# Optimization experiments

Hardware: AMD Instinct MI355X
Metric: run time of the kernel (lower is better)

## Reference

```python
import jax, jax.numpy as jnp
import numpy as np

N = 8192
IN_F = 512
NFEAT = 512
OUT_F = 512


def setup_inputs() -> dict:
    key = jax.random.key(0)
    k1, k2, k3, k4, k5 = jax.random.split(key, 5)
    stdv = 1.0 / np.sqrt(OUT_F)
    return {
        "input": jax.random.normal(k1, (N, IN_F), dtype=jnp.float32),
        "adj": jax.random.uniform(k2, (N, N), dtype=jnp.float32),
        "x": jax.random.normal(k3, (N, NFEAT), dtype=jnp.float32),
        "weight": jax.random.uniform(k4, (IN_F + N + NFEAT, OUT_F), minval=-stdv, maxval=stdv, dtype=jnp.float32),
        "bias": jax.random.uniform(k5, (OUT_F,), minval=-stdv, maxval=stdv, dtype=jnp.float32),
    }


def reference(input, adj, x, weight, bias):
    # support = [adj @ input | adj | x]  -> [n, in_features + n + nfeat]
    support = jnp.concatenate((adj @ input, adj, x), axis=1)
    return support @ weight + bias
```

## Files before the change

kernel.cpp:

```cpp
#include <hip/hip_runtime.h>
#include <hip/hip_bf16.h>

typedef __attribute__((ext_vector_type(4))) float f32x4;
typedef __attribute__((ext_vector_type(8))) short bf16x8;
typedef __attribute__((ext_vector_type(4))) unsigned short u16x4;
typedef __attribute__((ext_vector_type(8))) unsigned short u16x8;

__device__ __forceinline__ unsigned short f2bf(float f) {
    unsigned int u = __builtin_bit_cast(unsigned int, f);
    u += 0x7fffu + ((u >> 16) & 1u);
    return (unsigned short)(u >> 16);
}

#define SWZ(i) ((i) ^ ((((i) >> 6) & 7) << 3))

__global__ void transpose_cvt(const float* __restrict__ src,
                              unsigned short* __restrict__ dst,
                              int rows, int cols) {
    int idx = blockIdx.x * 256 + threadIdx.x;
    int n = idx / rows;
    int k = idx - n * rows;
    unsigned short v = f2bf(src[(size_t)k * cols + n]);
    int tile = (n >> 7) * (rows >> 6) + (k >> 6);
    dst[(size_t)tile * 8192 + SWZ((n & 127) * 64 + (k & 63))] = v;
}

template<int EPI>
__global__ __launch_bounds__(512, 4)
void gemm_small(const float* __restrict__ A, long lda,
                const unsigned short* __restrict__ Bt,
                int K,
                const float* __restrict__ epi, long lde,
                const float* __restrict__ bias,
                void* __restrict__ Dptr, long ldd) {
    __shared__ unsigned short sA[2][64 * 64];
    __shared__ unsigned short sB[2][128 * 64];

    const int t = threadIdx.x;
    const int l = t & 63;
    const int w = t >> 6;
    const int wm = w >> 2;
    const int wn = w & 3;

    int mt, nt;
    {
        int lin = blockIdx.y * gridDim.x + blockIdx.x;
        int xcd = lin & 7;
        int slot = lin >> 3;
        int ppx = gridDim.y >> 3;
        mt = xcd * ppx + slot / gridDim.x;
        nt = slot % gridDim.x;
    }
    const long m0 = (long)mt * 64;
    const long n0 = (long)nt * 128;
    const int KT = K >> 6;
    const unsigned short* Bblk = Bt + (size_t)nt * KT * 8192;

    f32x4 acc[2][2];
    #pragma unroll
    for (int m = 0; m < 2; ++m)
        #pragma unroll
        for (int n = 0; n < 2; ++n)
            acc[m][n] = {0.f, 0.f, 0.f, 0.f};

    f32x4 aX0, aX1, aY0, aY1;

    auto gll_B = [&](int kt, int buf) {
        const unsigned short* src = Bblk + (size_t)kt * 8192 + t * 8;
        #pragma unroll
        for (int r = 0; r < 2; ++r)
            __builtin_amdgcn_global_load_lds(
                (const __attribute__((address_space(1))) void*)(src + r * 4096),
                (__attribute__((address_space(3))) void*)&sB[buf][r * 4096 + w * 512],
                16, 0, 0);
    };

    auto load_A = [&](int kt, f32x4& a0, f32x4& a1) {
        const float* p0 = &A[(m0 + (t >> 4)) * lda + (long)kt * 64 + ((t & 15) << 2)];
        const float* p1 = p0 + 32 * lda;
        asm volatile("global_load_dwordx4 %0, %2, off\n\t"
                     "global_load_dwordx4 %1, %3, off"
                     : "=&v"(a0), "=&v"(a1)
                     : "v"(p0), "v"(p1)
                     : "memory");
    };

    auto write_A = [&](int buf, const f32x4& a0, const f32x4& a1) {
        int e0 = t * 4;
        u16x4 w0 = {f2bf(a0[0]), f2bf(a0[1]), f2bf(a0[2]), f2bf(a0[3])};
        *reinterpret_cast<u16x4*>(&sA[buf][SWZ(e0)]) = w0;
        int e1 = 2048 + t * 4;
        u16x4 w1 = {f2bf(a1[0]), f2bf(a1[1]), f2bf(a1[2]), f2bf(a1[3])};
        *reinterpret_cast<u16x4*>(&sA[buf][SWZ(e1)]) = w1;
    };

    auto compute = [&](int buf) {
        #pragma unroll
        for (int kk = 0; kk < 2; ++kk) {
            bf16x8 af[2], bfr[2];
            const int kb = kk * 32 + ((l >> 4) << 3);
            #pragma unroll
            for (int m = 0; m < 2; ++m) {
                int row = wm * 32 + m * 16 + (l & 15);
                af[m] = *reinterpret_cast<const bf16x8*>(&sA[buf][SWZ(row * 64 + kb)]);
            }
            #pragma unroll
            for (int n = 0; n < 2; ++n) {
                int col = wn * 32 + n * 16 + (l & 15);
                bfr[n] = *reinterpret_cast<const bf16x8*>(&sB[buf][SWZ(col * 64 + kb)]);
            }
            __builtin_amdgcn_s_setprio(1);
            #pragma unroll
            for (int m = 0; m < 2; ++m)
                #pragma unroll
                for (int n = 0; n < 2; ++n)
                    acc[m][n] = __builtin_amdgcn_mfma_f32_16x16x32_bf16(
                        af[m], bfr[n], acc[m][n], 0, 0, 0);
            __builtin_amdgcn_s_setprio(0);
        }
    };

    gll_B(0, 0);
    load_A(0, aX0, aX1);
    load_A(1, aY0, aY1);
    asm volatile("s_waitcnt vmcnt(2)" ::: "memory");
    __builtin_amdgcn_sched_barrier(0);
    write_A(0, aX0, aX1);
    asm volatile("s_waitcnt lgkmcnt(0)" ::: "memory");
    __builtin_amdgcn_s_barrier();
    __builtin_amdgcn_sched_barrier(0);

    const int nk = K >> 6;
    for (int p = 0; p + 2 < nk; p += 2) {
        gll_B(p + 1, 1);
        load_A(p + 2, aX0, aX1);
        compute(0);
        asm volatile("s_waitcnt vmcnt(4)" ::: "memory");
        __builtin_amdgcn_sched_barrier(0);
        write_A(1, aY0, aY1);
        asm volatile("s_waitcnt vmcnt(2) lgkmcnt(0)" ::: "memory");
        __builtin_amdgcn_s_barrier();
        __builtin_amdgcn_sched_barrier(0);

        gll_B(p + 2, 0);
        load_A(p + 3, aY0, aY1);
        compute(1);
        asm volatile("s_waitcnt vmcnt(4)" ::: "memory");
        __builtin_amdgcn_sched_barrier(0);
        write_A(0, aX0, aX1);
        asm volatile("s_waitcnt vmcnt(2) lgkmcnt(0)" ::: "memory");
        __builtin_amdgcn_s_barrier();
        __builtin_amdgcn_sched_barrier(0);
    }

    gll_B(nk - 1, 1);
    compute(0);
    asm volatile("s_waitcnt vmcnt(2)" ::: "memory");
    __builtin_amdgcn_sched_barrier(0);
    write_A(1, aY0, aY1);
    asm volatile("s_waitcnt vmcnt(0) lgkmcnt(0)" ::: "memory");
    __builtin_amdgcn_s_barrier();
    __builtin_amdgcn_sched_barrier(0);
    compute(1);

    const int jrow = (l >> 4) * 4;
    #pragma unroll
    for (int m = 0; m < 2; ++m) {
        const long row = m0 + wm * 32 + m * 16 + jrow;
        #pragma unroll
        for (int n = 0; n < 2; ++n) {
            const long col = n0 + wn * 32 + n * 16 + (l & 15);
            f32x4 v = acc[m][n];
            if constexpr (EPI == 0) {
                u16x4 o;
                #pragma unroll
                for (int j = 0; j < 4; ++j)
                    o[j] = f2bf(v[j] + epi[(row + j) * lde + col]);
                int tile = ((int)col >> 8) * 256 + ((int)row >> 5);
                int e = ((int)col & 255) * 32 + ((int)row & 31);
                *reinterpret_cast<u16x4*>(
                    &((unsigned short*)Dptr)[(size_t)tile * 8192 + SWZ(e)]) = o;
            } else {
                float b = bias[col];
                #pragma unroll
                for (int j = 0; j < 4; ++j)
                    ((float*)Dptr)[(row + j) * ldd + col] = v[j] + b;
            }
        }
    }
}

__global__ __launch_bounds__(512, 4)
void gemm_big(const float* __restrict__ A,
              const unsigned short* __restrict__ Bt,
              float* __restrict__ Out) {
    __shared__ unsigned short sA[2][128 * 32];
    __shared__ unsigned short sB[2][256 * 32];

    const int t = threadIdx.x;
    const int l = t & 63;
    const int w = t >> 6;
    const int wm = w & 1;
    const int wn = w >> 1;

    const int lin = blockIdx.x;
    const int xcd = lin & 7;
    const int idx = lin >> 3;
    const int mt = xcd * 8 + (idx & 7);
    const int rest = idx >> 3;
    const int nt = rest & 1;
    const int kq = rest >> 1;

    const long m0 = (long)mt * 128;
    const long k0 = (long)kq * 2048;
    const int ktb = nt * 256 + kq * 64;
    constexpr int P = 64;

    f32x4 acc[4][4];
    #pragma unroll
    for (int mi = 0; mi < 4; ++mi)
        #pragma unroll
        for (int ni = 0; ni < 4; ++ni)
            acc[mi][ni] = {0.f, 0.f, 0.f, 0.f};

    f32x4 aX0, aX1, aY0, aY1;

    auto gll_B = [&](int p, int buf) {
        const unsigned short* src = Bt + (size_t)(ktb + p) * 8192 + t * 8;
        #pragma unroll
        for (int r = 0; r < 2; ++r)
            __builtin_amdgcn_global_load_lds(
                (const __attribute__((address_space(1))) void*)(src + r * 4096),
                (__attribute__((address_space(3))) void*)&sB[buf][r * 4096 + w * 512],
                16, 0, 0);
    };

    auto load_A = [&](int p, f32x4& a0, f32x4& a1) {
        const float* base = A + m0 * 8192 + k0 + (long)p * 32;
        const float* p0 = base + (long)(t >> 3) * 8192 + ((t & 7) << 2);
        const float* p1 = base + (long)(64 + (t >> 3)) * 8192 + ((t & 7) << 2);
        asm volatile("global_load_dwordx4 %0, %2, off\n\t"
                     "global_load_dwordx4 %1, %3, off"
                     : "=&v"(a0), "=&v"(a1)
                     : "v"(p0), "v"(p1)
                     : "memory");
    };

    auto write_A = [&](int buf, const f32x4& a0, const f32x4& a1) {
        int e0 = (t >> 3) * 32 + ((t & 7) << 2);
        int e1 = (64 + (t >> 3)) * 32 + ((t & 7) << 2);
        u16x4 w0 = {f2bf(a0[0]), f2bf(a0[1]), f2bf(a0[2]), f2bf(a0[3])};
        *reinterpret_cast<u16x4*>(&sA[buf][SWZ(e0)]) = w0;
        u16x4 w1 = {f2bf(a1[0]), f2bf(a1[1]), f2bf(a1[2]), f2bf(a1[3])};
        *reinterpret_cast<u16x4*>(&sA[buf][SWZ(e1)]) = w1;
    };

    auto compute = [&](int buf) {
        const int kb = (l >> 4) << 3;
        bf16x8 af[4], bfr[4];
        #pragma unroll
        for (int mi = 0; mi < 4; ++mi) {
            int row = wm * 64 + mi * 16 + (l & 15);
            af[mi] = *reinterpret_cast<const bf16x8*>(&sA[buf][SWZ(row * 32 + kb)]);
        }
        #pragma unroll
        for (int ni = 0; ni < 4; ++ni) {
            int col = wn * 64 + ni * 16 + (l & 15);
            bfr[ni] = *reinterpret_cast<const bf16x8*>(&sB[buf][SWZ(col * 32 + kb)]);
        }
        __builtin_amdgcn_s_setprio(1);
        #pragma unroll
        for (int mi = 0; mi < 4; ++mi)
            #pragma unroll
            for (int ni = 0; ni < 4; ++ni)
                acc[mi][ni] = __builtin_amdgcn_mfma_f32_16x16x32_bf16(
                    af[mi], bfr[ni], acc[mi][ni], 0, 0, 0);
        __builtin_amdgcn_s_setprio(0);
    };

    gll_B(0, 0);
    load_A(0, aX0, aX1);
    load_A(1, aY0, aY1);
    asm volatile("s_waitcnt vmcnt(2)" ::: "memory");
    __builtin_amdgcn_sched_barrier(0);
    write_A(0, aX0, aX1);
    asm volatile("s_waitcnt lgkmcnt(0)" ::: "memory");
    __builtin_amdgcn_s_barrier();
    __builtin_amdgcn_sched_barrier(0);

    for (int p = 0; p + 2 < P; p += 2) {
        gll_B(p + 1, 1);
        load_A(p + 2, aX0, aX1);
        asm volatile("s_waitcnt vmcnt(4)" ::: "memory");
        __builtin_amdgcn_sched_barrier(0);
        write_A(1, aY0, aY1);
        compute(0);
        asm volatile("s_waitcnt vmcnt(2) lgkmcnt(0)" ::: "memory");
        __builtin_amdgcn_s_barrier();
        __builtin_amdgcn_sched_barrier(0);

        gll_B(p + 2, 0);
        load_A(p + 3, aY0, aY1);
        asm volatile("s_waitcnt vmcnt(4)" ::: "memory");
        __builtin_amdgcn_sched_barrier(0);
        write_A(0, aX0, aX1);
        compute(1);
        asm volatile("s_waitcnt vmcnt(2) lgkmcnt(0)" ::: "memory");
        __builtin_amdgcn_s_barrier();
        __builtin_amdgcn_sched_barrier(0);
    }

    gll_B(P - 1, 1);
    asm volatile("s_waitcnt vmcnt(2)" ::: "memory");
    __builtin_amdgcn_sched_barrier(0);
    write_A(1, aY0, aY1);
    compute(0);
    asm volatile("s_waitcnt vmcnt(0) lgkmcnt(0)" ::: "memory");
    __builtin_amdgcn_s_barrier();
    __builtin_amdgcn_sched_barrier(0);

    compute(1);

    #pragma unroll
    for (int mi = 0; mi < 4; ++mi) {
        const long row0 = m0 + wm * 64 + mi * 16 + ((l >> 4) << 2);
        #pragma unroll
        for (int ni = 0; ni < 4; ++ni) {
            const int col = nt * 256 + wn * 64 + ni * 16 + (l & 15);
            #pragma unroll
            for (int j = 0; j < 4; ++j)
                unsafeAtomicAdd(&Out[(row0 + j) * 512 + col], acc[mi][ni][j]);
        }
    }
}

extern "C" void kernel_launch(void* const* d_in, const int* in_sizes, int n_in,
                              void* d_out, int out_size, void* d_ws, size_t ws_size,
                              hipStream_t stream) {
    const float* input  = (const float*)d_in[0];
    const float* adj    = (const float*)d_in[1];
    const float* x      = (const float*)d_in[2];
    const float* weight = (const float*)d_in[3];
    const float* bias   = (const float*)d_in[4];

    const int N = 8192, IN_F = 512, NFEAT = 512, OUT_F = 512;
    float* out = (float*)d_out;

    unsigned short* Tbt = (unsigned short*)d_ws;
    unsigned short* W1t = Tbt + (size_t)OUT_F * N;
    unsigned short* W3t = W1t + (size_t)OUT_F * IN_F;

    transpose_cvt<<<dim3((IN_F * OUT_F) / 256), dim3(256), 0, stream>>>(
        weight, W1t, IN_F, OUT_F);
    transpose_cvt<<<dim3((NFEAT * OUT_F) / 256), dim3(256), 0, stream>>>(
        weight + (size_t)(IN_F + N) * OUT_F, W3t, NFEAT, OUT_F);

    dim3 grid(OUT_F / 128, N / 64);

    gemm_small<1><<<grid, 512, 0, stream>>>(
        x, (long)NFEAT, W3t, NFEAT,
        nullptr, 0, bias,
        out, (long)OUT_F);

    gemm_small<0><<<grid, 512, 0, stream>>>(
        input, (long)IN_F, W1t, IN_F,
        weight + (size_t)IN_F * OUT_F, (long)OUT_F, nullptr,
        Tbt, 0);

    gemm_big<<<dim3(512), dim3(512), 0, stream>>>(adj, Tbt, out);
}
```

Baseline: 172.7 us.

## Deepen gemm_big pipeline to triple-buffered B and three A register stages

```diff
diff --git a/kernel.cpp b/kernel.cpp
--- a/kernel.cpp
+++ b/kernel.cpp
@@ -195,7 +195,7 @@
               const unsigned short* __restrict__ Bt,
               float* __restrict__ Out) {
     __shared__ unsigned short sA[2][128 * 32];
-    __shared__ unsigned short sB[2][256 * 32];
+    __shared__ unsigned short sB[3][256 * 32];
 
     const int t = threadIdx.x;
     const int l = t & 63;
@@ -223,7 +223,7 @@
         for (int ni = 0; ni < 4; ++ni)
             acc[mi][ni] = {0.f, 0.f, 0.f, 0.f};
 
-    f32x4 aX0, aX1, aY0, aY1;
+    f32x4 a00, a01, a10, a11, a20, a21;
 
     auto gll_B = [&](int p, int buf) {
         const unsigned short* src = Bt + (size_t)(ktb + p) * 8192 + t * 8;
@@ -235,38 +235,38 @@
                 16, 0, 0);
     };
 
-    auto load_A = [&](int p, f32x4& a0, f32x4& a1) {
+    auto load_A = [&](int p, f32x4& x0, f32x4& x1) {
         const float* base = A + m0 * 8192 + k0 + (long)p * 32;
         const float* p0 = base + (long)(t >> 3) * 8192 + ((t & 7) << 2);
         const float* p1 = base + (long)(64 + (t >> 3)) * 8192 + ((t & 7) << 2);
         asm volatile("global_load_dwordx4 %0, %2, off\n\t"
                      "global_load_dwordx4 %1, %3, off"
-                     : "=&v"(a0), "=&v"(a1)
+                     : "=&v"(x0), "=&v"(x1)
                      : "v"(p0), "v"(p1)
                      : "memory");
     };
 
-    auto write_A = [&](int buf, const f32x4& a0, const f32x4& a1) {
+    auto write_A = [&](int buf, const f32x4& x0, const f32x4& x1) {
         int e0 = (t >> 3) * 32 + ((t & 7) << 2);
         int e1 = (64 + (t >> 3)) * 32 + ((t & 7) << 2);
-        u16x4 w0 = {f2bf(a0[0]), f2bf(a0[1]), f2bf(a0[2]), f2bf(a0[3])};
+        u16x4 w0 = {f2bf(x0[0]), f2bf(x0[1]), f2bf(x0[2]), f2bf(x0[3])};
         *reinterpret_cast<u16x4*>(&sA[buf][SWZ(e0)]) = w0;
-        u16x4 w1 = {f2bf(a1[0]), f2bf(a1[1]), f2bf(a1[2]), f2bf(a1[3])};
+        u16x4 w1 = {f2bf(x1[0]), f2bf(x1[1]), f2bf(x1[2]), f2bf(x1[3])};
         *reinterpret_cast<u16x4*>(&sA[buf][SWZ(e1)]) = w1;
     };
 
-    auto compute = [&](int buf) {
+    auto compute = [&](int bufA, int bufB) {
         const int kb = (l >> 4) << 3;
         bf16x8 af[4], bfr[4];
         #pragma unroll
         for (int mi = 0; mi < 4; ++mi) {
             int row = wm * 64 + mi * 16 + (l & 15);
-            af[mi] = *reinterpret_cast<const bf16x8*>(&sA[buf][SWZ(row * 32 + kb)]);
+            af[mi] = *reinterpret_cast<const bf16x8*>(&sA[bufA][SWZ(row * 32 + kb)]);
         }
         #pragma unroll
         for (int ni = 0; ni < 4; ++ni) {
             int col = wn * 64 + ni * 16 + (l & 15);
-            bfr[ni] = *reinterpret_cast<const bf16x8*>(&sB[buf][SWZ(col * 32 + kb)]);
+            bfr[ni] = *reinterpret_cast<const bf16x8*>(&sB[bufB][SWZ(col * 32 + kb)]);
         }
         __builtin_amdgcn_s_setprio(1);
         #pragma unroll
@@ -278,48 +278,67 @@
         __builtin_amdgcn_s_setprio(0);
     };
 
+    load_A(0, a00, a01);
     gll_B(0, 0);
-    load_A(0, aX0, aX1);
-    load_A(1, aY0, aY1);
     asm volatile("s_waitcnt vmcnt(2)" ::: "memory");
     __builtin_amdgcn_sched_barrier(0);
-    write_A(0, aX0, aX1);
-    asm volatile("s_waitcnt lgkmcnt(0)" ::: "memory");
-    __builtin_amdgcn_s_barrier();
-    __builtin_amdgcn_sched_barrier(0);
-
-    for (int p = 0; p + 2 < P; p += 2) {
-        gll_B(p + 1, 1);
-        load_A(p + 2, aX0, aX1);
-        asm volatile("s_waitcnt vmcnt(4)" ::: "memory");
-        __builtin_amdgcn_sched_barrier(0);
-        write_A(1, aY0, aY1);
-        compute(0);
-        asm volatile("s_waitcnt vmcnt(2) lgkmcnt(0)" ::: "memory");
-        __builtin_amdgcn_s_barrier();
-        __builtin_amdgcn_sched_barrier(0);
-
-        gll_B(p + 2, 0);
-        load_A(p + 3, aY0, aY1);
-        asm volatile("s_waitcnt vmcnt(4)" ::: "memory");
-        __builtin_amdgcn_sched_barrier(0);
-        write_A(0, aX0, aX1);
-        compute(1);
-        asm volatile("s_waitcnt vmcnt(2) lgkmcnt(0)" ::: "memory");
-        __builtin_amdgcn_s_barrier();
-        __builtin_amdgcn_sched_barrier(0);
-    }
-
-    gll_B(P - 1, 1);
+    write_A(0, a00, a01);
+    load_A(1, a10, a11);
+    gll_B(1, 1);
+    load_A(2, a20, a21);
+    asm volatile("s_waitcnt vmcnt(6) lgkmcnt(0)" ::: "memory");
+    __builtin_amdgcn_s_barrier();
+    __builtin_amdgcn_sched_barrier(0);
+
+#define PHASE_FULL(Pexpr, SAW, SAC, BB, BC, L0, L1, W0, W1)                   \
+    gll_B((Pexpr) + 2, BB);                                                   \
+    load_A((Pexpr) + 3, L0, L1);                                              \
+    asm volatile("s_waitcnt vmcnt(8)" ::: "memory");                          \
+    __builtin_amdgcn_sched_barrier(0);                                        \
+    write_A(SAW, W0, W1);                                                     \
+    compute(SAC, BC);                                                         \
+    asm volatile("s_waitcnt vmcnt(6) lgkmcnt(0)" ::: "memory");               \
+    __builtin_amdgcn_s_barrier();                                             \
+    __builtin_amdgcn_sched_barrier(0);
+
+    for (int p = 0; p < P - 4; p += 6) {
+        PHASE_FULL(p + 0, 1, 0, 2, 0, a00, a01, a10, a11)
+        PHASE_FULL(p + 1, 0, 1, 0, 1, a10, a11, a20, a21)
+        PHASE_FULL(p + 2, 1, 0, 1, 2, a20, a21, a00, a01)
+        PHASE_FULL(p + 3, 0, 1, 2, 0, a00, a01, a10, a11)
+        PHASE_FULL(p + 4, 1, 0, 0, 1, a10, a11, a20, a21)
+        PHASE_FULL(p + 5, 0, 1, 1, 2, a20, a21, a00, a01)
+    }
+#undef PHASE_FULL
+
+    gll_B(62, 2);
+    load_A(63, a00, a01);
+    asm volatile("s_waitcnt vmcnt(8)" ::: "memory");
+    __builtin_amdgcn_sched_barrier(0);
+    write_A(1, a10, a11);
+    compute(0, 0);
+    asm volatile("s_waitcnt vmcnt(6) lgkmcnt(0)" ::: "memory");
+    __builtin_amdgcn_s_barrier();
+    __builtin_amdgcn_sched_barrier(0);
+
+    gll_B(63, 0);
+    asm volatile("s_waitcnt vmcnt(6)" ::: "memory");
+    __builtin_amdgcn_sched_barrier(0);
+    write_A(0, a20, a21);
+    compute(1, 1);
+    asm volatile("s_waitcnt vmcnt(4) lgkmcnt(0)" ::: "memory");
+    __builtin_amdgcn_s_barrier();
+    __builtin_amdgcn_sched_barrier(0);
+
     asm volatile("s_waitcnt vmcnt(2)" ::: "memory");
     __builtin_amdgcn_sched_barrier(0);
-    write_A(1, aY0, aY1);
-    compute(0);
+    write_A(1, a00, a01);
+    compute(0, 2);
     asm volatile("s_waitcnt vmcnt(0) lgkmcnt(0)" ::: "memory");
     __builtin_amdgcn_s_barrier();
     __builtin_amdgcn_sched_barrier(0);
 
-    compute(1);
+    compute(1, 0);
 
     #pragma unroll
     for (int mi = 0; mi < 4; ++mi) {
```

After: 186.9 us. +8.2%, slower.

## Load A fragments directly from global into registers, deepen K step per stage

Applied to the files above, without the earlier changes.

```diff
diff --git a/kernel.cpp b/kernel.cpp
--- a/kernel.cpp
+++ b/kernel.cpp
@@ -194,14 +194,13 @@
 void gemm_big(const float* __restrict__ A,
               const unsigned short* __restrict__ Bt,
               float* __restrict__ Out) {
-    __shared__ unsigned short sA[2][128 * 32];
-    __shared__ unsigned short sB[2][256 * 32];
+    __shared__ unsigned short sB[2][2 * 8192];
 
     const int t = threadIdx.x;
     const int l = t & 63;
     const int w = t >> 6;
-    const int wm = w & 1;
-    const int wn = w >> 1;
+    const int wm = w >> 1;
+    const int wn = w & 1;
 
     const int lin = blockIdx.x;
     const int xcd = lin & 7;
@@ -214,119 +213,97 @@
     const long m0 = (long)mt * 128;
     const long k0 = (long)kq * 2048;
     const int ktb = nt * 256 + kq * 64;
-    constexpr int P = 64;
-
-    f32x4 acc[4][4];
+    constexpr int P = 32;
+
+    f32x4 acc[2][8];
     #pragma unroll
-    for (int mi = 0; mi < 4; ++mi)
-        #pragma unroll
-        for (int ni = 0; ni < 4; ++ni)
+    for (int mi = 0; mi < 2; ++mi)
+        #pragma unroll
+        for (int ni = 0; ni < 8; ++ni)
             acc[mi][ni] = {0.f, 0.f, 0.f, 0.f};
 
-    f32x4 aX0, aX1, aY0, aY1;
-
     auto gll_B = [&](int p, int buf) {
-        const unsigned short* src = Bt + (size_t)(ktb + p) * 8192 + t * 8;
-        #pragma unroll
-        for (int r = 0; r < 2; ++r)
-            __builtin_amdgcn_global_load_lds(
-                (const __attribute__((address_space(1))) void*)(src + r * 4096),
-                (__attribute__((address_space(3))) void*)&sB[buf][r * 4096 + w * 512],
-                16, 0, 0);
-    };
-
-    auto load_A = [&](int p, f32x4& a0, f32x4& a1) {
-        const float* base = A + m0 * 8192 + k0 + (long)p * 32;
-        const float* p0 = base + (long)(t >> 3) * 8192 + ((t & 7) << 2);
-        const float* p1 = base + (long)(64 + (t >> 3)) * 8192 + ((t & 7) << 2);
-        asm volatile("global_load_dwordx4 %0, %2, off\n\t"
-                     "global_load_dwordx4 %1, %3, off"
-                     : "=&v"(a0), "=&v"(a1)
-                     : "v"(p0), "v"(p1)
-                     : "memory");
-    };
-
-    auto write_A = [&](int buf, const f32x4& a0, const f32x4& a1) {
-        int e0 = (t >> 3) * 32 + ((t & 7) << 2);
-        int e1 = (64 + (t >> 3)) * 32 + ((t & 7) << 2);
-        u16x4 w0 = {f2bf(a0[0]), f2bf(a0[1]), f2bf(a0[2]), f2bf(a0[3])};
-        *reinterpret_cast<u16x4*>(&sA[buf][SWZ(e0)]) = w0;
-        u16x4 w1 = {f2bf(a1[0]), f2bf(a1[1]), f2bf(a1[2]), f2bf(a1[3])};
-        *reinterpret_cast<u16x4*>(&sA[buf][SWZ(e1)]) = w1;
-    };
-
-    auto compute = [&](int buf) {
+        #pragma unroll
+        for (int sub = 0; sub < 2; ++sub) {
+            const unsigned short* src =
+                Bt + (size_t)(ktb + 2 * p + sub) * 8192 + t * 8;
+            #pragma unroll
+            for (int r = 0; r < 2; ++r)
+                __builtin_amdgcn_global_load_lds(
+                    (const __attribute__((address_space(1))) void*)(src + r * 4096),
+                    (__attribute__((address_space(3))) void*)
+                        &sB[buf][sub * 8192 + r * 4096 + w * 512],
+                    16, 0, 0);
+        }
+    };
+
+    const long rowA0 = m0 + wm * 32 + (l & 15);
+    const float* aRow0 = A + rowA0 * 8192 + k0 + ((l >> 4) << 3);
+    const float* aRow1 = aRow0 + 16 * 8192;
+
+    auto compute = [&](int p, int buf) {
         const int kb = (l >> 4) << 3;
-        bf16x8 af[4], bfr[4];
-        #pragma unroll
-        for (int mi = 0; mi < 4; ++mi) {
-            int row = wm * 64 + mi * 16 + (l & 15);
-            af[mi] = *reinterpret_cast<const bf16x8*>(&sA[buf][SWZ(row * 32 + kb)]);
-        }
-        #pragma unroll
-        for (int ni = 0; ni < 4; ++ni) {
-            int col = wn * 64 + ni * 16 + (l & 15);
-            bfr[ni] = *reinterpret_cast<const bf16x8*>(&sB[buf][SWZ(col * 32 + kb)]);
-        }
-        __builtin_amdgcn_s_setprio(1);
-        #pragma unroll
-        for (int mi = 0; mi < 4; ++mi)
-            #pragma unroll
-            for (int ni = 0; ni < 4; ++ni)
-                acc[mi][ni] = __builtin_amdgcn_mfma_f32_16x16x32_bf16(
-                    af[mi], bfr[ni], acc[mi][ni], 0, 0, 0);
-        __builtin_amdgcn_s_setprio(0);
+        f32x4 r00a = *reinterpret_cast<const f32x4*>(aRow0 + (long)p * 64);
+        f32x4 r00b = *reinterpret_cast<const f32x4*>(aRow0 + (long)p * 64 + 4);
+        f32x4 r01a = *reinterpret_cast<const f32x4*>(aRow0 + (long)p * 64 + 32);
+        f32x4 r01b = *reinterpret_cast<const f32x4*>(aRow0 + (long)p * 64 + 36);
+        f32x4 r10a = *reinterpret_cast<const f32x4*>(aRow1 + (long)p * 64);
+        f32x4 r10b = *reinterpret_cast<const f32x4*>(aRow1 + (long)p * 64 + 4);
+        f32x4 r11a = *reinterpret_cast<const f32x4*>(aRow1 + (long)p * 64 + 32);
+        f32x4 r11b = *reinterpret_cast<const f32x4*>(aRow1 + (long)p * 64 + 36);
+
+        auto cvt = [&](const f32x4& a, const f32x4& b) -> bf16x8 {
+            u16x8 o;
+            o[0] = f2bf(a[0]); o[1] = f2bf(a[1]); o[2] = f2bf(a[2]); o[3] = f2bf(a[3]);
+            o[4] = f2bf(b[0]); o[5] = f2bf(b[1]); o[6] = f2bf(b[2]); o[7] = f2bf(b[3]);
+            return __builtin_bit_cast(bf16x8, o);
+        };
+        bf16x8 af[2][2];
+        af[0][0] = cvt(r00a, r00b);
+        af[0][1] = cvt(r01a, r01b);
+        af[1][0] = cvt(r10a, r10b);
+        af[1][1] = cvt(r11a, r11b);
+
+        #pragma unroll
+        for (int kk = 0; kk < 2; ++kk) {
+            bf16x8 bfr[8];
+            #pragma unroll
+            for (int ni = 0; ni < 8; ++ni) {
+                int col = wn * 128 + ni * 16 + (l & 15);
+                bfr[ni] = *reinterpret_cast<const bf16x8*>(
+                    &sB[buf][kk * 8192 + SWZ(col * 32 + kb)]);
+            }
+            __builtin_amdgcn_s_setprio(1);
+            #pragma unroll
+            for (int mi = 0; mi < 2; ++mi)
+                #pragma unroll
+                for (int ni = 0; ni < 8; ++ni)
+                    acc[mi][ni] = __builtin_amdgcn_mfma_f32_16x16x32_bf16(
+                        af[mi][kk], bfr[ni], acc[mi][ni], 0, 0, 0);
+            __builtin_amdgcn_s_setprio(0);
+        }
     };
 
     gll_B(0, 0);
-    load_A(0, aX0, aX1);
-    load_A(1, aY0, aY1);
-    asm volatile("s_waitcnt vmcnt(2)" ::: "memory");
-    __builtin_amdgcn_sched_barrier(0);
-    write_A(0, aX0, aX1);
-    asm volatile("s_waitcnt lgkmcnt(0)" ::: "memory");
-    __builtin_amdgcn_s_barrier();
-    __builtin_amdgcn_sched_barrier(0);
-
-    for (int p = 0; p + 2 < P; p += 2) {
-        gll_B(p + 1, 1);
-        load_A(p + 2, aX0, aX1);
-        asm volatile("s_waitcnt vmcnt(4)" ::: "memory");
-        __builtin_amdgcn_sched_barrier(0);
-        write_A(1, aY0, aY1);
-        compute(0);
-        asm volatile("s_waitcnt vmcnt(2) lgkmcnt(0)" ::: "memory");
-        __builtin_amdgcn_s_barrier();
-        __builtin_amdgcn_sched_barrier(0);
-
-        gll_B(p + 2, 0);
-        load_A(p + 3, aY0, aY1);
-        asm volatile("s_waitcnt vmcnt(4)" ::: "memory");
-        __builtin_amdgcn_sched_barrier(0);
-        write_A(0, aX0, aX1);
-        compute(1);
-        asm volatile("s_waitcnt vmcnt(2) lgkmcnt(0)" ::: "memory");
-        __builtin_amdgcn_s_barrier();
-        __builtin_amdgcn_sched_barrier(0);
-    }
-
-    gll_B(P - 1, 1);
-    asm volatile("s_waitcnt vmcnt(2)" ::: "memory");
-    __builtin_amdgcn_sched_barrier(0);
-    write_A(1, aY0, aY1);
-    compute(0);
     asm volatile("s_waitcnt vmcnt(0) lgkmcnt(0)" ::: "memory");
     __builtin_amdgcn_s_barrier();
     __builtin_amdgcn_sched_barrier(0);
 
-    compute(1);
+    for (int p = 0; p < P - 1; ++p) {
+        gll_B(p + 1, (p + 1) & 1);
+        compute(p, p & 1);
+        asm volatile("s_waitcnt vmcnt(0) lgkmcnt(0)" ::: "memory");
+        __builtin_amdgcn_s_barrier();
+        __builtin_amdgcn_sched_barrier(0);
+    }
+    compute(P - 1, (P - 1) & 1);
 
     #pragma unroll
-    for (int mi = 0; mi < 4; ++mi) {
-        const long row0 = m0 + wm * 64 + mi * 16 + ((l >> 4) << 2);
-        #pragma unroll
-        for (int ni = 0; ni < 4; ++ni) {
-            const int col = nt * 256 + wn * 64 + ni * 16 + (l & 15);
+    for (int mi = 0; mi < 2; ++mi) {
+        const long row0 = m0 + wm * 32 + mi * 16 + ((l >> 4) << 2);
+        #pragma unroll
+        for (int ni = 0; ni < 8; ++ni) {
+            const int col = nt * 256 + wn * 128 + ni * 16 + (l & 15);
             #pragma unroll
             for (int j = 0; j < 4; ++j)
                 unsafeAtomicAdd(&Out[(row0 + j) * 512 + col], acc[mi][ni][j]);
```

New measurement: 399.0 us. 2.31x slower.
